# Kernel tuning notes

Hardware: AMD Instinct MI355X
Metric: run time of the kernel (lower is better)

## Reference

```python
import jax, jax.numpy as jnp
import numpy as np

D_MODEL = 1024
N_HEADS = 16
D_K = D_MODEL // N_HEADS
D_FF = 4096
B, S = 2, 2048
LN_EPS = 1e-5
NEG_INF = -1e30  # finite stand-in for -inf; first (all-masked) row is overwritten by zeros anyway


def layer_norm(x, g, b):
    mu = jnp.mean(x, axis=-1, keepdims=True)
    var = jnp.mean(jnp.square(x - mu), axis=-1, keepdims=True)
    return (x - mu) * jax.lax.rsqrt(var + LN_EPS) * g + b


def setup_inputs() -> dict:
    key = jax.random.key(0)
    ks = jax.random.split(key, 16)
    sd = 0.02
    inp = {
        "query": jax.random.normal(ks[0], (B, S, D_MODEL), jnp.float32),
        "key": jax.random.normal(ks[1], (B, S, D_MODEL), jnp.float32),
        "values": jax.random.normal(ks[2], (B, S, D_MODEL), jnp.float32),
        "Wq": jax.random.normal(ks[3], (D_MODEL, D_MODEL), jnp.float32) * sd,
        "bq": jnp.zeros((D_MODEL,), jnp.float32),
        "Wk": jax.random.normal(ks[4], (D_MODEL, D_MODEL), jnp.float32) * sd,
        "bk": jnp.zeros((D_MODEL,), jnp.float32),
        "Wv": jax.random.normal(ks[5], (D_MODEL, D_MODEL), jnp.float32) * sd,
        "bv": jnp.zeros((D_MODEL,), jnp.float32),
        "Wo": jax.random.normal(ks[6], (D_MODEL, D_MODEL), jnp.float32) * sd,
        "bo": jnp.zeros((D_MODEL,), jnp.float32),
        "ln1_g": jnp.ones((D_MODEL,), jnp.float32),
        "ln1_b": jnp.zeros((D_MODEL,), jnp.float32),
        "W1": jax.random.normal(ks[7], (D_MODEL, D_FF), jnp.float32) * sd,
        "b1": jnp.zeros((D_FF,), jnp.float32),
        "W2": jax.random.normal(ks[8], (D_FF, D_MODEL), jnp.float32) * sd,
        "b2": jnp.zeros((D_MODEL,), jnp.float32),
        "ln2_g": jnp.ones((D_MODEL,), jnp.float32),
        "ln2_b": jnp.zeros((D_MODEL,), jnp.float32),
        "mask": 0,
    }
    return inp


def reference(query, key, values, Wq, bq, Wk, bk, Wv, bv, Wo, bo,
              ln1_g, ln1_b, W1, b1, W2, b2, ln2_g, ln2_b, mask):
    b, s, d = query.shape
    # projections -> [B, H, S, d_k]
    q = (query @ Wq + bq).reshape(b, s, N_HEADS, D_K).transpose(0, 2, 1, 3)
    k = (key @ Wk + bk).reshape(b, s, N_HEADS, D_K).transpose(0, 2, 1, 3)
    v = (values @ Wv + bv).reshape(b, s, N_HEADS, D_K).transpose(0, 2, 1, 3)
    # scores [B, H, S, S]
    scores = jnp.einsum("bhqd,bhkd->bhqk", q, k) / jnp.sqrt(jnp.float32(D_K))
    # torch: triu(ones, k=mask)==0 -> allowed iff j < i + mask
    i = jnp.arange(s)[:, None]
    j = jnp.arange(s)[None, :]
    allowed = j < (i + mask)
    scores = jnp.where(allowed, scores, NEG_INF)
    attn = jax.nn.softmax(scores, axis=-1)
    if mask == 0:
        # zero-pad trick: first query row (fully masked) is replaced by zeros
        attn = attn.at[:, :, 0, :].set(0.0)
    ctx = jnp.einsum("bhqk,bhkd->bhqd", attn, v)
    ctx = ctx.transpose(0, 2, 1, 3).reshape(b, s, d)
    attn_out = ctx @ Wo + bo
    x = layer_norm(query + attn_out, ln1_g, ln1_b)
    ffn = jax.nn.relu(x @ W1 + b1) @ W2 + b2
    out = layer_norm(x + ffn, ln2_g, ln2_b)
    return out
```

## Files before the change

### kernel.cpp

```cpp
#include <hip/hip_runtime.h>


typedef __attribute__((ext_vector_type(8))) __bf16 bf16x8;
typedef __attribute__((ext_vector_type(4))) float f32x4;
typedef __attribute__((ext_vector_type(8))) short s16x8;

struct alignas(8)  S4 { short x, y, z, w; };
struct alignas(16) F4 { float x, y, z, w; };
struct alignas(16) I4 { int x, y, z, w; };

static __device__ __forceinline__ short f2bf(float f) {
  unsigned u = __float_as_uint(f);
  u += 0x7fff + ((u >> 16) & 1);
  return (short)(u >> 16);
}

static __device__ __forceinline__ void store_out(float* p, float v) { *p = v; }
static __device__ __forceinline__ void store_out(short* p, float v) { *p = f2bf(v); }

#define GLL16(g, l)                                                         \
  __builtin_amdgcn_global_load_lds(                                         \
      (__attribute__((address_space(1))) void*)(g),                         \
      (__attribute__((address_space(3))) void*)(l), 16, 0, 0)

__global__ __launch_bounds__(256) void cvt_bf16_kernel(
    const float* __restrict__ i0, const float* __restrict__ i1,
    const float* __restrict__ i2, short* __restrict__ o0,
    short* __restrict__ o1, short* __restrict__ o2) {
  int z = blockIdx.y;
  const float* in = z == 0 ? i0 : (z == 1 ? i1 : i2);
  short* out = z == 0 ? o0 : (z == 1 ? o1 : o2);
  int i = (blockIdx.x * 256 + threadIdx.x) * 4;
  F4 v = *(const F4*)(in + i);
  S4 o = { f2bf(v.x), f2bf(v.y), f2bf(v.z), f2bf(v.w) };
  *(S4*)(out + i) = o;
}

__global__ __launch_bounds__(256) void transpose_cvt_kernel(
    const float* __restrict__ Wq, const float* __restrict__ Wk,
    const float* __restrict__ Wv, const float* __restrict__ Wo,
    const float* __restrict__ W1, const float* __restrict__ W2,
    short* __restrict__ Wqt, short* __restrict__ Wkt,
    short* __restrict__ Wvt, short* __restrict__ Wot,
    short* __restrict__ W1t, short* __restrict__ W2t) {
  __shared__ float tile[64][65];
  int bid = blockIdx.x;
  const float* W; short* Wt; int K, N, kx, ny;
  if (bid < 1024) {
    int w = bid >> 8, t = bid & 255;
    W = w == 0 ? Wq : (w == 1 ? Wk : (w == 2 ? Wv : Wo));
    Wt = w == 0 ? Wqt : (w == 1 ? Wkt : (w == 2 ? Wvt : Wot));
    K = 1024; N = 1024; kx = t & 15; ny = t >> 4;
  } else if (bid < 2048) {
    int t = bid - 1024;
    W = W1; Wt = W1t; K = 1024; N = 4096; kx = t & 15; ny = t >> 4;
  } else {
    int t = bid - 2048;
    W = W2; Wt = W2t; K = 4096; N = 1024; kx = t & 63; ny = t >> 6;
  }
  int k0 = kx * 64, n0 = ny * 64;
  int tid = threadIdx.x;
  int rr = tid >> 4, cc = (tid & 15) * 4;
#pragma unroll
  for (int p = 0; p < 4; ++p) {
    int row = p * 16 + rr;
    F4 v = *(const F4*)&W[(long)(k0 + row) * N + n0 + cc];
    tile[row][cc] = v.x; tile[row][cc + 1] = v.y;
    tile[row][cc + 2] = v.z; tile[row][cc + 3] = v.w;
  }
  __syncthreads();
#pragma unroll
  for (int p = 0; p < 4; ++p) {
    int rn = p * 16 + rr;
    S4 o = { f2bf(tile[cc + 0][rn]), f2bf(tile[cc + 1][rn]),
             f2bf(tile[cc + 2][rn]), f2bf(tile[cc + 3][rn]) };
    *(S4*)&Wt[(long)(n0 + rn) * K + k0 + cc] = o;
  }
}

template <int OUT_MODE, bool RELU, bool RES, typename OT>
__device__ __forceinline__ void gemm_core(
    const short* __restrict__ A, const short* __restrict__ Bt,
    const float* __restrict__ bias, const float* __restrict__ res,
    OT* __restrict__ out, int M, int N, int K, int kBeg, int kEnd) {
  __shared__ __align__(16) short sA[128 * 64];
  __shared__ __align__(16) short sB[128 * 64];
  int tid = threadIdx.x;
  int lane = tid & 63, wave = tid >> 6;
  int col = lane & 15, quad = lane >> 4;
  int m0 = blockIdx.x * 128, n0 = blockIdx.y * 128;
  int wm = (wave & 1) * 64, wn = (wave >> 1) * 64;

  f32x4 acc[4][4] = {};

  for (int k0 = kBeg; k0 < kEnd; k0 += 64) {
    __syncthreads();
#pragma unroll
    for (int j = 0; j < 4; ++j) {
      int idx = j * 256 + tid;
      int row = idx >> 3, cp = idx & 7;
      int c = cp ^ (row & 7);
      const short* ga = A  + (long)(m0 + row) * K + k0 + c * 8;
      const short* gb = Bt + (long)(n0 + row) * K + k0 + c * 8;
      short* la = &sA[(j * 256 + (wave << 6)) * 8];
      short* lb = &sB[(j * 256 + (wave << 6)) * 8];
      GLL16(ga, la);
      GLL16(gb, lb);
    }
    __syncthreads();

#pragma unroll
    for (int kk = 0; kk < 2; ++kk) {
      bf16x8 a[4], b[4];
#pragma unroll
      for (int t = 0; t < 4; ++t) {
        int ra = wm + t * 16 + col;
        int ca = kk * 4 + quad;
        a[t] = *(const bf16x8*)&sA[ra * 64 + ((ca ^ (ra & 7)) << 3)];
        int rb = wn + t * 16 + col;
        b[t] = *(const bf16x8*)&sB[rb * 64 + ((ca ^ (rb & 7)) << 3)];
      }
#pragma unroll
      for (int t = 0; t < 4; ++t)
#pragma unroll
        for (int u = 0; u < 4; ++u)
          acc[t][u] = __builtin_amdgcn_mfma_f32_16x16x32_bf16(
              a[t], b[u], acc[t][u], 0, 0, 0);
    }
  }

#pragma unroll
  for (int t = 0; t < 4; ++t) {
#pragma unroll
    for (int u = 0; u < 4; ++u) {
      int Cc = n0 + wn + u * 16 + col;
      float bv = bias ? bias[Cc] : 0.f;
#pragma unroll
      for (int r = 0; r < 4; ++r) {
        int R = m0 + wm + t * 16 + quad * 4 + r;
        float v = acc[t][u][r] + bv;
        if (RES) v += res[(long)R * N + Cc];
        if (RELU) v = v > 0.f ? v : 0.f;
        if (OUT_MODE == 0) {
          store_out(&out[(long)R * N + Cc], v);
        } else {
          int bb = R >> 11, s = R & 2047, h = Cc >> 6, d = Cc & 63;
          store_out(&out[((long)((bb * 16 + h) * 2048 + s) << 6) + d], v);
        }
      }
    }
  }
}

template <int OUT_MODE, bool RELU, bool RES, typename OT>
__global__ __launch_bounds__(256) void gemm_bt(
    const short* __restrict__ A, const short* __restrict__ Bt,
    const float* __restrict__ bias, const float* __restrict__ res,
    OT* __restrict__ out, int M, int N, int K) {
  gemm_core<OUT_MODE, RELU, RES, OT>(A, Bt, bias, res, out, M, N, K, 0, K);
}

__global__ __launch_bounds__(256) void gemm_splitk(
    const short* __restrict__ A, const short* __restrict__ Bt,
    const float* __restrict__ bias, float* __restrict__ p0,
    float* __restrict__ p1, int M, int N, int K) {
  int z = blockIdx.z;
  float* out = z == 0 ? p0 : p1;
  const float* b = z == 0 ? bias : nullptr;
  int kc = K >> 1;
  gemm_core<0, false, false, float>(A, Bt, b, nullptr, out, M, N, K,
                                    z * kc, z * kc + kc);
}

__global__ __launch_bounds__(256) void gemm_qkv(
    const short* __restrict__ Aq, const short* __restrict__ Ak,
    const short* __restrict__ Av, const short* __restrict__ Btq,
    const short* __restrict__ Btk, const short* __restrict__ Btv,
    const float* __restrict__ bq, const float* __restrict__ bk,
    const float* __restrict__ bv, short* __restrict__ Qp,
    short* __restrict__ Kp, short* __restrict__ Vp) {
  int z = blockIdx.z;
  const short* A = z == 0 ? Aq : (z == 1 ? Ak : Av);
  const short* Bt = z == 0 ? Btq : (z == 1 ? Btk : Btv);
  const float* bias = z == 0 ? bq : (z == 1 ? bk : bv);
  short* out = z == 0 ? Qp : (z == 1 ? Kp : Vp);
  gemm_core<1, false, false, short>(A, Bt, bias, nullptr, out,
                                    4096, 1024, 1024, 0, 1024);
}

__global__ __launch_bounds__(256) void attn_kernel(
    const short* __restrict__ Q, const short* __restrict__ K,
    const short* __restrict__ V, const int* __restrict__ maskp,
    short* __restrict__ ctx) {
  __shared__ __align__(16) short sK[2][64 * 64];
  __shared__ __align__(16) int   sVt[2][64 * 32];
  __shared__ __align__(16) short sP[4 * 16 * 64];
  int tid = threadIdx.x, wave = tid >> 6;
  int lane = tid & 63;
  int col = lane & 15, quad = lane >> 4;
  int bh = blockIdx.x;
  int qt = 31 - blockIdx.y;
  int maskv = maskp[0];
  const long base = (long)bh * (2048 * 64);
  int b = bh >> 4, h = bh & 15;

  int kp = tid & 31, dg = tid >> 5, d0v = dg * 8;

  int i0 = qt * 64 + wave * 16;

  long jmax = (long)qt * 64 + 63 + maskv - 1;
  int tot = (jmax < 0) ? 0 : (int)(jmax >> 6) + 1;
  if (tot > 32) tot = 32;

  bf16x8 aQ[2];
#pragma unroll
  for (int kk = 0; kk < 2; ++kk)
    aQ[kk] = *(const bf16x8*)&Q[base + (long)(i0 + col) * 64 + kk * 32 + quad * 8];

  f32x4 o[4] = {};
  float lsum[4] = { 0.f, 0.f, 0.f, 0.f };

  if (tot > 0) {
#pragma unroll
    for (int j = 0; j < 2; ++j) {
      int idx = j * 256 + tid;
      int row = idx >> 3, cp = idx & 7;
      int c = cp ^ (row & 7);
      GLL16(K + base + (long)row * 64 + c * 8,
            &sK[0][(j * 256 + (wave << 6)) * 8]);
    }
    {
      s16x8 u0 = *(const s16x8*)&V[base + (long)(2 * kp) * 64 + d0v];
      s16x8 u1 = *(const s16x8*)&V[base + (long)(2 * kp + 1) * 64 + d0v];
#pragma unroll
      for (int j = 0; j < 8; ++j) {
        int d = d0v + j;
        int w = ((int)(unsigned short)u1[j] << 16) | (unsigned short)u0[j];
        sVt[0][d * 32 + ((((kp >> 2) ^ (d & 7)) << 2) | (kp & 3))] = w;
      }
    }
  }
  __syncthreads();

  for (int kt = 0; kt < tot; ++kt) {
    int cur = kt & 1, nxt = cur ^ 1;
    bool pf = (kt + 1 < tot);

    s16x8 u0, u1;
    if (pf) {
#pragma unroll
      for (int j = 0; j < 2; ++j) {
        int idx = j * 256 + tid;
        int row = idx >> 3, cp = idx & 7;
        int c = cp ^ (row & 7);
        GLL16(K + base + (long)((kt + 1) * 64 + row) * 64 + c * 8,
              &sK[nxt][(j * 256 + (wave << 6)) * 8]);
      }
      u0 = *(const s16x8*)&V[base + (long)((kt + 1) * 64 + 2 * kp) * 64 + d0v];
      u1 = *(const s16x8*)&V[base + (long)((kt + 1) * 64 + 2 * kp + 1) * 64 + d0v];
    }

    f32x4 sc[4] = {};
#pragma unroll
    for (int kk = 0; kk < 2; ++kk) {
      int ca = kk * 4 + quad;
#pragma unroll
      for (int nt = 0; nt < 4; ++nt) {
        int rk = nt * 16 + col;
        bf16x8 bK = *(const bf16x8*)&sK[cur][rk * 64 + ((ca ^ (rk & 7)) << 3)];
        sc[nt] = __builtin_amdgcn_mfma_f32_16x16x32_bf16(aQ[kk], bK, sc[nt], 0, 0, 0);
      }
    }

    bool interior = (kt * 64 + 63) < (i0 + maskv);
    if (interior) {
#pragma unroll
      for (int r = 0; r < 4; ++r) {
        int qr = quad * 4 + r;
#pragma unroll
        for (int nt = 0; nt < 4; ++nt) {
          float p = __expf(sc[nt][r] * 0.125f);
          lsum[r] += p;
          int k8 = nt * 2 + (col >> 3);
          sP[wave * 1024 + qr * 64 + (((k8 ^ (qr & 7)) << 3) | (col & 7))] =
              f2bf(p);
        }
      }
    } else {
#pragma unroll
      for (int r = 0; r < 4; ++r) {
        int i = i0 + quad * 4 + r;
        int qr = quad * 4 + r;
#pragma unroll
        for (int nt = 0; nt < 4; ++nt) {
          int j = kt * 64 + nt * 16 + col;
          float p = (j < i + maskv) ? __expf(sc[nt][r] * 0.125f) : 0.f;
          lsum[r] += p;
          int k8 = nt * 2 + (col >> 3);
          sP[wave * 1024 + qr * 64 + (((k8 ^ (qr & 7)) << 3) | (col & 7))] =
              f2bf(p);
        }
      }
    }

#pragma unroll
    for (int kk = 0; kk < 2; ++kk) {
      int ca = kk * 4 + quad;
      bf16x8 aP = *(const bf16x8*)&sP[wave * 1024 + col * 64 + ((ca ^ (col & 7)) << 3)];
#pragma unroll
      for (int dt = 0; dt < 4; ++dt) {
        int d = dt * 16 + col;
        bf16x8 bV = *(const bf16x8*)((const short*)sVt[cur] + d * 64 + ((ca ^ (d & 7)) << 3));
        o[dt] = __builtin_amdgcn_mfma_f32_16x16x32_bf16(aP, bV, o[dt], 0, 0, 0);
      }
    }

    if (pf) {
#pragma unroll
      for (int j = 0; j < 8; ++j) {
        int d = d0v + j;
        int w = ((int)(unsigned short)u1[j] << 16) | (unsigned short)u0[j];
        sVt[nxt][d * 32 + ((((kp >> 2) ^ (d & 7)) << 2) | (kp & 3))] = w;
      }
    }
    __syncthreads();
  }

#pragma unroll
  for (int r = 0; r < 4; ++r)
#pragma unroll
    for (int off = 1; off < 16; off <<= 1)
      lsum[r] += __shfl_xor(lsum[r], off);

#pragma unroll
  for (int r = 0; r < 4; ++r) {
    int i = i0 + quad * 4 + r;
    float inv = (lsum[r] > 0.f) ? 1.f / lsum[r] : 0.f;
    if (maskv == 0 && i == 0) inv = 0.f;
#pragma unroll
    for (int dt = 0; dt < 4; ++dt)
      ctx[(long)(b * 2048 + i) * 1024 + h * 64 + dt * 16 + col] =
          f2bf(o[dt][r] * inv);
  }
}

__global__ __launch_bounds__(256) void ln_comb_kernel(
    const float* __restrict__ p0, const float* __restrict__ p1,
    const float* __restrict__ res, const float* __restrict__ g,
    const float* __restrict__ b, float* __restrict__ outf,
    short* __restrict__ outb) {
  int r = blockIdx.x, tid = threadIdx.x;
  int lane = tid & 63, wave = tid >> 6;
  long off0 = (long)r * 1024;
  F4 a = ((const F4*)(p0 + off0))[tid];
  F4 c = ((const F4*)(p1 + off0))[tid];
  F4 d = ((const F4*)(res + off0))[tid];
  F4 v = { a.x + c.x + d.x, a.y + c.y + d.y, a.z + c.z + d.z, a.w + c.w + d.w };
  float s = v.x + v.y + v.z + v.w;
  float sq = v.x * v.x + v.y * v.y + v.z * v.z + v.w * v.w;
#pragma unroll
  for (int off = 1; off < 64; off <<= 1) {
    s += __shfl_xor(s, off);
    sq += __shfl_xor(sq, off);
  }
  __shared__ float rs[4], rq[4];
  if (lane == 0) { rs[wave] = s; rq[wave] = sq; }
  __syncthreads();
  s = rs[0] + rs[1] + rs[2] + rs[3];
  sq = rq[0] + rq[1] + rq[2] + rq[3];
  float mu = s * (1.0f / 1024.0f);
  float var = sq * (1.0f / 1024.0f) - mu * mu;
  float rstd = rsqrtf(var + 1e-5f);
  F4 gv = ((const F4*)g)[tid], bv = ((const F4*)b)[tid];
  F4 o;
  o.x = (v.x - mu) * rstd * gv.x + bv.x;
  o.y = (v.y - mu) * rstd * gv.y + bv.y;
  o.z = (v.z - mu) * rstd * gv.z + bv.z;
  o.w = (v.w - mu) * rstd * gv.w + bv.w;
  ((F4*)(outf + off0))[tid] = o;
  if (outb) {
    S4 ob = { f2bf(o.x), f2bf(o.y), f2bf(o.z), f2bf(o.w) };
    ((S4*)(outb + off0))[tid] = ob;
  }
}

extern "C" void kernel_launch(void* const* d_in, const int* in_sizes, int n_in,
                              void* d_out, int out_size, void* d_ws, size_t ws_size,
                              hipStream_t stream) {
  const float* query  = (const float*)d_in[0];
  const float* keyi   = (const float*)d_in[1];
  const float* values = (const float*)d_in[2];
  const float* Wq = (const float*)d_in[3];
  const float* bq = (const float*)d_in[4];
  const float* Wk = (const float*)d_in[5];
  const float* bk = (const float*)d_in[6];
  const float* Wv = (const float*)d_in[7];
  const float* bv = (const float*)d_in[8];
  const float* Wo = (const float*)d_in[9];
  const float* bo = (const float*)d_in[10];
  const float* ln1_g = (const float*)d_in[11];
  const float* ln1_b = (const float*)d_in[12];
  const float* W1 = (const float*)d_in[13];
  const float* b1 = (const float*)d_in[14];
  const float* W2 = (const float*)d_in[15];
  const float* b2 = (const float*)d_in[16];
  const float* ln2_g = (const float*)d_in[17];
  const float* ln2_b = (const float*)d_in[18];
  const int*   maskp = (const int*)d_in[19];
  float* out = (float*)d_out;

  char* ws = (char*)d_ws;
  const size_t MB = 1u << 20;
  short* q_bf = (short*)(ws + 0);
  short* k_bf = (short*)(ws + 8 * MB);
  short* v_bf = (short*)(ws + 16 * MB);
  short* ctx  = (short*)(ws + 24 * MB);
  short* Qp   = (short*)(ws + 32 * MB);
  short* Kp   = (short*)(ws + 40 * MB);
  short* Vp   = (short*)(ws + 48 * MB);
  short* Wqt  = (short*)(ws + 56 * MB);
  short* Wkt  = (short*)(ws + 58 * MB);
  short* Wvt  = (short*)(ws + 60 * MB);
  short* Wot  = (short*)(ws + 62 * MB);
  short* W1t  = (short*)(ws + 64 * MB);
  short* W2t  = (short*)(ws + 72 * MB);
  short* hbuf = (short*)(ws + 80 * MB);
  float* pWo0 = (float*)(ws + 0);
  float* pWo1 = (float*)(ws + 32 * MB);
  float* x_f32 = (float*)(ws + 16 * MB);
  short* x_bf  = (short*)(ws + 48 * MB);
  float* pF0 = (float*)(ws + 0);
  float* pF1 = (float*)(ws + 32 * MB);

  cvt_bf16_kernel<<<dim3(4096, 3), 256, 0, stream>>>(query, keyi, values,
                                                     q_bf, k_bf, v_bf);
  transpose_cvt_kernel<<<3072, 256, 0, stream>>>(Wq, Wk, Wv, Wo, W1, W2,
                                                 Wqt, Wkt, Wvt, Wot, W1t, W2t);
  gemm_qkv<<<dim3(32, 8, 3), 256, 0, stream>>>(q_bf, k_bf, v_bf,
                                               Wqt, Wkt, Wvt,
                                               bq, bk, bv, Qp, Kp, Vp);
  attn_kernel<<<dim3(32, 32), 256, 0, stream>>>(Qp, Kp, Vp, maskp, ctx);
  gemm_splitk<<<dim3(32, 8, 2), 256, 0, stream>>>(ctx, Wot, bo, pWo0, pWo1,
                                                  4096, 1024, 1024);
  ln_comb_kernel<<<4096, 256, 0, stream>>>(pWo0, pWo1, query, ln1_g, ln1_b,
                                           x_f32, x_bf);
  gemm_bt<0, true, false, short><<<dim3(32, 32), 256, 0, stream>>>(
      x_bf, W1t, b1, nullptr, hbuf, 4096, 4096, 1024);
  gemm_splitk<<<dim3(32, 8, 2), 256, 0, stream>>>(hbuf, W2t, b2, pF0, pF1,
                                                  4096, 1024, 4096);
  ln_comb_kernel<<<4096, 256, 0, stream>>>(pF0, pF1, x_f32, ln2_g, ln2_b,
                                           out, nullptr);

  (void)in_sizes; (void)n_in; (void)out_size; (void)ws_size;
}
```

Baseline: 397.9 us.

## Replace GEMMs with 256-tile double-buffered 8-wave pipelined kernel and set MFMA priorities

Replaces the 128x128 single-buffered GEMM core with a 256xBN tile kernel using 512 threads, double-buffered LDS, explicit vmcnt/lgkmcnt waits and staggered stage loads interleaved with MFMA phases. All four projection/FFN GEMMs now use it, with different grids, and s_setprio is added around MFMA blocks in both the GEMMs and attention. The aim is to overlap global loads with matrix math and raise data reuse per block, in exchange for fewer, larger blocks (possible tail/occupancy loss) and hand-tuned waitcnt counts that must match the issued loads exactly.

```diff
diff --git a/kernel.cpp b/kernel.cpp
--- a/kernel.cpp
+++ b/kernel.cpp
@@ -7,7 +7,6 @@
 
 struct alignas(8)  S4 { short x, y, z, w; };
 struct alignas(16) F4 { float x, y, z, w; };
-struct alignas(16) I4 { int x, y, z, w; };
 
 static __device__ __forceinline__ short f2bf(float f) {
   unsigned u = __float_as_uint(f);
@@ -78,68 +77,179 @@
   }
 }
 
-template <int OUT_MODE, bool RELU, bool RES, typename OT>
-__device__ __forceinline__ void gemm_core(
+template <int NF, int OUT_MODE, bool RELU, typename OT>
+__device__ __forceinline__ void gemm256_core(
     const short* __restrict__ A, const short* __restrict__ Bt,
-    const float* __restrict__ bias, const float* __restrict__ res,
-    OT* __restrict__ out, int M, int N, int K, int kBeg, int kEnd) {
-  __shared__ __align__(16) short sA[128 * 64];
-  __shared__ __align__(16) short sB[128 * 64];
+    const float* __restrict__ bias, OT* __restrict__ out,
+    int N, int K, int kBeg, int kEnd, int m0, int n0) {
+  constexpr int BN = NF * 64;
+  constexpr int LB = BN / 64;
+  __shared__ __align__(16) short sA[2][256 * 64];
+  __shared__ __align__(16) short sB[2][BN * 64];
   int tid = threadIdx.x;
   int lane = tid & 63, wave = tid >> 6;
   int col = lane & 15, quad = lane >> 4;
-  int m0 = blockIdx.x * 128, n0 = blockIdx.y * 128;
-  int wm = (wave & 1) * 64, wn = (wave >> 1) * 64;
-
-  f32x4 acc[4][4] = {};
-
-  for (int k0 = kBeg; k0 < kEnd; k0 += 64) {
-    __syncthreads();
+  int wm = (wave >> 2) * 128;
+  int wn = (wave & 3) * (NF * 16);
+
+  f32x4 acc[8][NF] = {};
+
+  const int NT = (kEnd - kBeg) >> 6;
+  const int t0 = kBeg >> 6;
+
+  auto stageA = [&](int buf, int kt) {
 #pragma unroll
     for (int j = 0; j < 4; ++j) {
-      int idx = j * 256 + tid;
+      int idx = j * 512 + tid;
       int row = idx >> 3, cp = idx & 7;
       int c = cp ^ (row & 7);
-      const short* ga = A  + (long)(m0 + row) * K + k0 + c * 8;
-      const short* gb = Bt + (long)(n0 + row) * K + k0 + c * 8;
-      short* la = &sA[(j * 256 + (wave << 6)) * 8];
-      short* lb = &sB[(j * 256 + (wave << 6)) * 8];
-      GLL16(ga, la);
-      GLL16(gb, lb);
-    }
-    __syncthreads();
-
-#pragma unroll
-    for (int kk = 0; kk < 2; ++kk) {
-      bf16x8 a[4], b[4];
-#pragma unroll
-      for (int t = 0; t < 4; ++t) {
-        int ra = wm + t * 16 + col;
+      GLL16(A + (long)(m0 + row) * K + kt * 64 + c * 8,
+            &sA[buf][(j * 512 + (wave << 6)) * 8]);
+    }
+  };
+  auto stageB = [&](int buf, int kt) {
+#pragma unroll
+    for (int j = 0; j < LB; ++j) {
+      int idx = j * 512 + tid;
+      int row = idx >> 3, cp = idx & 7;
+      int c = cp ^ (row & 7);
+      GLL16(Bt + (long)(n0 + row) * K + kt * 64 + c * 8,
+            &sB[buf][(j * 512 + (wave << 6)) * 8]);
+    }
+  };
+
+  stageA(0, t0);     stageB(0, t0);
+  stageA(1, t0 + 1); stageB(1, t0 + 1);
+  if constexpr (NF == 4) asm volatile("s_waitcnt vmcnt(8)" ::: "memory");
+  else                   asm volatile("s_waitcnt vmcnt(6)" ::: "memory");
+  __builtin_amdgcn_sched_barrier(0);
+  __builtin_amdgcn_s_barrier();
+
+  for (int t = 0; t < NT; ++t) {
+    int cur = t & 1;
+    bool pf = (t + 2 < NT);
+    bf16x8 bf[NF][2], af[2][2];
+
+#pragma unroll
+    for (int n = 0; n < NF; ++n) {
+      int rb = wn + n * 16 + col;
+#pragma unroll
+      for (int kk = 0; kk < 2; ++kk) {
         int ca = kk * 4 + quad;
-        a[t] = *(const bf16x8*)&sA[ra * 64 + ((ca ^ (ra & 7)) << 3)];
-        int rb = wn + t * 16 + col;
-        b[t] = *(const bf16x8*)&sB[rb * 64 + ((ca ^ (rb & 7)) << 3)];
-      }
-#pragma unroll
-      for (int t = 0; t < 4; ++t)
-#pragma unroll
-        for (int u = 0; u < 4; ++u)
-          acc[t][u] = __builtin_amdgcn_mfma_f32_16x16x32_bf16(
-              a[t], b[u], acc[t][u], 0, 0, 0);
-    }
-  }
-
-#pragma unroll
-  for (int t = 0; t < 4; ++t) {
-#pragma unroll
-    for (int u = 0; u < 4; ++u) {
-      int Cc = n0 + wn + u * 16 + col;
+        bf[n][kk] = *(const bf16x8*)&sB[cur][rb * 64 + ((ca ^ (rb & 7)) << 3)];
+      }
+    }
+#pragma unroll
+    for (int i = 0; i < 2; ++i) {
+      int ra = wm + i * 16 + col;
+#pragma unroll
+      for (int kk = 0; kk < 2; ++kk) {
+        int ca = kk * 4 + quad;
+        af[i][kk] = *(const bf16x8*)&sA[cur][ra * 64 + ((ca ^ (ra & 7)) << 3)];
+      }
+    }
+    asm volatile("s_waitcnt lgkmcnt(0)" ::: "memory");
+    __builtin_amdgcn_sched_barrier(0);
+    __builtin_amdgcn_s_setprio(1);
+#pragma unroll
+    for (int i = 0; i < 2; ++i)
+#pragma unroll
+      for (int n = 0; n < NF; ++n)
+#pragma unroll
+        for (int kk = 0; kk < 2; ++kk)
+          acc[i][n] = __builtin_amdgcn_mfma_f32_16x16x32_bf16(
+              af[i][kk], bf[n][kk], acc[i][n], 0, 0, 0);
+    __builtin_amdgcn_s_setprio(0);
+    __builtin_amdgcn_s_barrier();
+    __builtin_amdgcn_sched_barrier(0);
+
+    if (pf) stageB(cur, t0 + t + 2);
+#pragma unroll
+    for (int i = 0; i < 2; ++i) {
+      int ra = wm + (2 + i) * 16 + col;
+#pragma unroll
+      for (int kk = 0; kk < 2; ++kk) {
+        int ca = kk * 4 + quad;
+        af[i][kk] = *(const bf16x8*)&sA[cur][ra * 64 + ((ca ^ (ra & 7)) << 3)];
+      }
+    }
+    __builtin_amdgcn_s_setprio(1);
+#pragma unroll
+    for (int i = 0; i < 2; ++i)
+#pragma unroll
+      for (int n = 0; n < NF; ++n)
+#pragma unroll
+        for (int kk = 0; kk < 2; ++kk)
+          acc[2 + i][n] = __builtin_amdgcn_mfma_f32_16x16x32_bf16(
+              af[i][kk], bf[n][kk], acc[2 + i][n], 0, 0, 0);
+    __builtin_amdgcn_s_setprio(0);
+    __builtin_amdgcn_s_barrier();
+
+#pragma unroll
+    for (int i = 0; i < 2; ++i) {
+      int ra = wm + (4 + i) * 16 + col;
+#pragma unroll
+      for (int kk = 0; kk < 2; ++kk) {
+        int ca = kk * 4 + quad;
+        af[i][kk] = *(const bf16x8*)&sA[cur][ra * 64 + ((ca ^ (ra & 7)) << 3)];
+      }
+    }
+    __builtin_amdgcn_s_setprio(1);
+#pragma unroll
+    for (int i = 0; i < 2; ++i)
+#pragma unroll
+      for (int n = 0; n < NF; ++n)
+#pragma unroll
+        for (int kk = 0; kk < 2; ++kk)
+          acc[4 + i][n] = __builtin_amdgcn_mfma_f32_16x16x32_bf16(
+              af[i][kk], bf[n][kk], acc[4 + i][n], 0, 0, 0);
+    __builtin_amdgcn_s_setprio(0);
+    __builtin_amdgcn_s_barrier();
+
+#pragma unroll
+    for (int i = 0; i < 2; ++i) {
+      int ra = wm + (6 + i) * 16 + col;
+#pragma unroll
+      for (int kk = 0; kk < 2; ++kk) {
+        int ca = kk * 4 + quad;
+        af[i][kk] = *(const bf16x8*)&sA[cur][ra * 64 + ((ca ^ (ra & 7)) << 3)];
+      }
+    }
+    asm volatile("s_waitcnt lgkmcnt(0)" ::: "memory");
+    __builtin_amdgcn_sched_barrier(0);
+    __builtin_amdgcn_s_barrier();
+    __builtin_amdgcn_sched_barrier(0);
+    if (pf) stageA(cur, t0 + t + 2);
+    __builtin_amdgcn_s_setprio(1);
+#pragma unroll
+    for (int i = 0; i < 2; ++i)
+#pragma unroll
+      for (int n = 0; n < NF; ++n)
+#pragma unroll
+        for (int kk = 0; kk < 2; ++kk)
+          acc[6 + i][n] = __builtin_amdgcn_mfma_f32_16x16x32_bf16(
+              af[i][kk], bf[n][kk], acc[6 + i][n], 0, 0, 0);
+    __builtin_amdgcn_s_setprio(0);
+    if (pf) {
+      if constexpr (NF == 4) asm volatile("s_waitcnt vmcnt(8)" ::: "memory");
+      else                   asm volatile("s_waitcnt vmcnt(6)" ::: "memory");
+    } else {
+      asm volatile("s_waitcnt vmcnt(0)" ::: "memory");
+    }
+    __builtin_amdgcn_sched_barrier(0);
+    __builtin_amdgcn_s_barrier();
+  }
+
+#pragma unroll
+  for (int m = 0; m < 8; ++m) {
+#pragma unroll
+    for (int n = 0; n < NF; ++n) {
+      int Cc = n0 + wn + n * 16 + col;
       float bv = bias ? bias[Cc] : 0.f;
 #pragma unroll
       for (int r = 0; r < 4; ++r) {
-        int R = m0 + wm + t * 16 + quad * 4 + r;
-        float v = acc[t][u][r] + bv;
-        if (RES) v += res[(long)R * N + Cc];
+        int R = m0 + wm + m * 16 + quad * 4 + r;
+        float v = acc[m][n][r] + bv;
         if (RELU) v = v > 0.f ? v : 0.f;
         if (OUT_MODE == 0) {
           store_out(&out[(long)R * N + Cc], v);
@@ -152,27 +262,14 @@
   }
 }
 
-template <int OUT_MODE, bool RELU, bool RES, typename OT>
-__global__ __launch_bounds__(256) void gemm_bt(
+__global__ __launch_bounds__(512) void g256_ffn1(
     const short* __restrict__ A, const short* __restrict__ Bt,
-    const float* __restrict__ bias, const float* __restrict__ res,
-    OT* __restrict__ out, int M, int N, int K) {
-  gemm_core<OUT_MODE, RELU, RES, OT>(A, Bt, bias, res, out, M, N, K, 0, K);
-}
-
-__global__ __launch_bounds__(256) void gemm_splitk(
-    const short* __restrict__ A, const short* __restrict__ Bt,
-    const float* __restrict__ bias, float* __restrict__ p0,
-    float* __restrict__ p1, int M, int N, int K) {
-  int z = blockIdx.z;
-  float* out = z == 0 ? p0 : p1;
-  const float* b = z == 0 ? bias : nullptr;
-  int kc = K >> 1;
-  gemm_core<0, false, false, float>(A, Bt, b, nullptr, out, M, N, K,
-                                    z * kc, z * kc + kc);
-}
-
-__global__ __launch_bounds__(256) void gemm_qkv(
+    const float* __restrict__ bias, short* __restrict__ out) {
+  gemm256_core<4, 0, true, short>(A, Bt, bias, out, 4096, 1024, 0, 1024,
+                                  blockIdx.x * 256, blockIdx.y * 256);
+}
+
+__global__ __launch_bounds__(512) void g256_qkv(
     const short* __restrict__ Aq, const short* __restrict__ Ak,
     const short* __restrict__ Av, const short* __restrict__ Btq,
     const short* __restrict__ Btk, const short* __restrict__ Btv,
@@ -184,8 +281,32 @@
   const short* Bt = z == 0 ? Btq : (z == 1 ? Btk : Btv);
   const float* bias = z == 0 ? bq : (z == 1 ? bk : bv);
   short* out = z == 0 ? Qp : (z == 1 ? Kp : Vp);
-  gemm_core<1, false, false, short>(A, Bt, bias, nullptr, out,
-                                    4096, 1024, 1024, 0, 1024);
+  gemm256_core<4, 1, false, short>(A, Bt, bias, out, 1024, 1024, 0, 1024,
+                                   blockIdx.x * 256, blockIdx.y * 256);
+}
+
+__global__ __launch_bounds__(512) void g256_wo(
+    const short* __restrict__ A, const short* __restrict__ Bt,
+    const float* __restrict__ bias, float* __restrict__ p0,
+    float* __restrict__ p1) {
+  int z = blockIdx.z;
+  float* out = z == 0 ? p0 : p1;
+  const float* b = z == 0 ? bias : nullptr;
+  gemm256_core<2, 0, false, float>(A, Bt, b, out, 1024, 1024,
+                                   z * 512, z * 512 + 512,
+                                   blockIdx.x * 256, blockIdx.y * 128);
+}
+
+__global__ __launch_bounds__(512) void g256_ffn2(
+    const short* __restrict__ A, const short* __restrict__ Bt,
+    const float* __restrict__ bias, float* __restrict__ p0,
+    float* __restrict__ p1) {
+  int z = blockIdx.z;
+  float* out = z == 0 ? p0 : p1;
+  const float* b = z == 0 ? bias : nullptr;
+  gemm256_core<2, 0, false, float>(A, Bt, b, out, 1024, 4096,
+                                   z * 2048, z * 2048 + 2048,
+                                   blockIdx.x * 256, blockIdx.y * 128);
 }
 
 __global__ __launch_bounds__(256) void attn_kernel(
@@ -261,6 +382,7 @@
     }
 
     f32x4 sc[4] = {};
+    __builtin_amdgcn_s_setprio(1);
 #pragma unroll
     for (int kk = 0; kk < 2; ++kk) {
       int ca = kk * 4 + quad;
@@ -271,6 +393,7 @@
         sc[nt] = __builtin_amdgcn_mfma_f32_16x16x32_bf16(aQ[kk], bK, sc[nt], 0, 0, 0);
       }
     }
+    __builtin_amdgcn_s_setprio(0);
 
     bool interior = (kt * 64 + 63) < (i0 + maskv);
     if (interior) {
@@ -303,6 +426,7 @@
       }
     }
 
+    __builtin_amdgcn_s_setprio(1);
 #pragma unroll
     for (int kk = 0; kk < 2; ++kk) {
       int ca = kk * 4 + quad;
@@ -314,6 +438,7 @@
         o[dt] = __builtin_amdgcn_mfma_f32_16x16x32_bf16(aP, bV, o[dt], 0, 0, 0);
       }
     }
+    __builtin_amdgcn_s_setprio(0);
 
     if (pf) {
 #pragma unroll
@@ -436,18 +561,15 @@
                                                      q_bf, k_bf, v_bf);
   transpose_cvt_kernel<<<3072, 256, 0, stream>>>(Wq, Wk, Wv, Wo, W1, W2,
                                                  Wqt, Wkt, Wvt, Wot, W1t, W2t);
-  gemm_qkv<<<dim3(32, 8, 3), 256, 0, stream>>>(q_bf, k_bf, v_bf,
+  g256_qkv<<<dim3(16, 4, 3), 512, 0, stream>>>(q_bf, k_bf, v_bf,
                                                Wqt, Wkt, Wvt,
                                                bq, bk, bv, Qp, Kp, Vp);
   attn_kernel<<<dim3(32, 32), 256, 0, stream>>>(Qp, Kp, Vp, maskp, ctx);
-  gemm_splitk<<<dim3(32, 8, 2), 256, 0, stream>>>(ctx, Wot, bo, pWo0, pWo1,
-                                                  4096, 1024, 1024);
+  g256_wo<<<dim3(16, 8, 2), 512, 0, stream>>>(ctx, Wot, bo, pWo0, pWo1);
   ln_comb_kernel<<<4096, 256, 0, stream>>>(pWo0, pWo1, query, ln1_g, ln1_b,
                                            x_f32, x_bf);
-  gemm_bt<0, true, false, short><<<dim3(32, 32), 256, 0, stream>>>(
-      x_bf, W1t, b1, nullptr, hbuf, 4096, 4096, 1024);
-  gemm_splitk<<<dim3(32, 8, 2), 256, 0, stream>>>(hbuf, W2t, b2, pF0, pF1,
-                                                  4096, 1024, 4096);
+  g256_ffn1<<<dim3(16, 16), 512, 0, stream>>>(x_bf, W1t, b1, hbuf);
+  g256_ffn2<<<dim3(16, 8, 2), 512, 0, stream>>>(hbuf, W2t, b2, pF0, pF1);
   ln_comb_kernel<<<4096, 256, 0, stream>>>(pF0, pF1, x_f32, ln2_g, ln2_b,
                                            out, nullptr);
 
```

Result: faster. 383.0 us (-3.7%).
